# Kernel tuning notes

Measured on AMD Instinct MI355X. Metric: run time of the kernel, lower is better.

Reference implementation:

```python
import jax, jax.numpy as jnp
import numpy as np

N_NODES = 50000
N_EDGES = 800000
D_IN = 96
D_OUT = 96


def setup_inputs() -> dict:
    key = jax.random.key(0)
    k1, k2, k3 = jax.random.split(key, 3)
    x = jax.random.normal(k1, (N_NODES, D_IN), dtype=jnp.float32)
    edge_index = jax.random.randint(k2, (2, N_EDGES), 0, N_NODES, dtype=jnp.int64)
    edge_weight = jnp.ones((N_EDGES,), dtype=jnp.float32)
    # Glorot-ish init for the linear weight, zero bias (as in PyG GCNConv)
    W = jax.random.normal(k3, (D_IN, D_OUT), dtype=jnp.float32) * (1.0 / np.sqrt(D_IN))
    b = jnp.zeros((D_OUT,), dtype=jnp.float32)
    return {"x": x, "edge_index": edge_index, "edge_weight": edge_weight, "W": W, "b": b}


def reference(x, edge_index, edge_weight, W, b):
    """PyG GCNConv: out = D^{-1/2} (A + I) D^{-1/2} (x @ W) + b."""
    N = x.shape[0]
    row, col = edge_index[0], edge_index[1]  # source -> target
    # add self loops with weight 1 (PyG default add_self_loops=True)
    loop = jnp.arange(N, dtype=edge_index.dtype)
    row = jnp.concatenate([row, loop])
    col = jnp.concatenate([col, loop])
    ew = jnp.concatenate([edge_weight, jnp.ones((N,), dtype=edge_weight.dtype)])
    # symmetric normalization based on (weighted) in-degree over col
    deg = jax.ops.segment_sum(ew, col, num_segments=N)  # [N]
    dinv = jnp.where(deg > 0, jax.lax.rsqrt(deg), 0.0)
    norm = dinv[row] * ew * dinv[col]  # [E+N]
    # linear transform first (small GEMM), then gather-scale-scatter over edges
    h = x @ W  # [N, D_OUT]
    msg = h[row] * norm[:, None]  # [E+N, D_OUT]
    out = jax.ops.segment_sum(msg, col, num_segments=N)  # [N, D_OUT]
    return out + b
```

## Files before the change

### kernel.cpp

```cpp
#include <hip/hip_runtime.h>

#define N_NODES 50000
#define N_EDGES 800000
#define D 96
#define NBKT 256
#define BNODES 196
#define BCAP 4608
#define PART_B 250
#define EPB (N_EDGES / PART_B)
#define EPT 13
#define CAP 48
#define NSLOT (BNODES * CAP)
#define KDUMP 37
#define GCAP 768

typedef float vfloat4 __attribute__((ext_vector_type(4)));

__device__ __forceinline__ float bf_lo(unsigned u) { return __uint_as_float(u << 16); }
__device__ __forceinline__ float bf_hi(unsigned u) { return __uint_as_float(u & 0xFFFF0000u); }
__device__ __forceinline__ unsigned f2bf_bits(unsigned u) {
    return (u + 0x7FFFu + ((u >> 16) & 1u)) & 0xFFFF0000u;
}

__device__ __forceinline__ int exscan256(int v, int* wsum) {
    int lane = threadIdx.x & 63;
    int wave = threadIdx.x >> 6;
    int incl = v;
#pragma unroll
    for (int off = 1; off < 64; off <<= 1) {
        int t = __shfl_up(incl, off);
        if (lane >= off) incl += t;
    }
    if (lane == 63) wsum[wave] = incl;
    __syncthreads();
    int base = 0;
#pragma unroll
    for (int wv = 0; wv < 3; ++wv) base += (wv < wave) ? wsum[wv] : 0;
    return base + incl - v;
}

__global__ __launch_bounds__(256) void k_part(const int* __restrict__ row,
                                              const int* __restrict__ col,
                                              const float* __restrict__ ew,
                                              int* __restrict__ bkt_cnt,
                                              uint2* __restrict__ bktbuf) {
    __shared__ int hist[NBKT];
    __shared__ int cur[NBKT];
    int tid = threadIdx.x;
    hist[tid] = 0;
    __syncthreads();
    int e0 = blockIdx.x * EPB;

    int myc[EPT];
#pragma unroll
    for (int k = 0; k < EPT; ++k) {
        int i = tid + 256 * k;
        myc[k] = (i < EPB) ? col[e0 + i] : -1;
    }
#pragma unroll
    for (int k = 0; k < EPT; ++k)
        if (myc[k] >= 0) atomicAdd(&hist[myc[k] / BNODES], 1);
    __syncthreads();
    cur[tid] = atomicAdd(&bkt_cnt[tid], hist[tid]);
    __syncthreads();
#pragma unroll
    for (int k = 0; k < EPT; ++k) {
        int i = tid + 256 * k;
        if (myc[k] >= 0) {
            int e = e0 + i;
            int c = myc[k];
            int b = c / BNODES;
            int p = atomicAdd(&cur[b], 1);
            if (p < BCAP)
                bktbuf[(size_t)b * BCAP + p] =
                    make_uint2((unsigned)row[e] | ((unsigned)(c - b * BNODES) << 16),
                               __float_as_uint(ew[e]));
        }
    }
}

__global__ __launch_bounds__(256) void k_bin(const int* __restrict__ bkt_cnt,
                                             const uint2* __restrict__ bktbuf,
                                             unsigned* __restrict__ recs,
                                             int* __restrict__ rowptr,
                                             float* __restrict__ dinv) {
    __shared__ int wsum1[4];
    __shared__ int wsum2[4];
    __shared__ int sbkt[NBKT];
    __shared__ int lcnt[BNODES];
    __shared__ int loff[256];
    __shared__ int stot;
    __shared__ unsigned lslot[NSLOT];
    int tid = threadIdx.x;
    int b = blockIdx.x;

    int bv = min(bkt_cnt[tid], BCAP);
    int bex = exscan256(bv, wsum1);
    sbkt[tid] = bex;
    for (int i = tid; i < BNODES; i += 256) lcnt[i] = 0;
    __syncthreads();
    int gbase = sbkt[b];
    int ne = min(bkt_cnt[b], BCAP);

    for (int i = tid; i < ne; i += 256) {
        uint2 r = bktbuf[(size_t)b * BCAP + i];
        int lc = (int)(r.x >> 16);
        int p = atomicAdd(&lcnt[lc], 1);
        if (p < CAP) lslot[lc * CAP + p] = f2bf_bits(r.y) | (r.x & 0xFFFFu);
    }
    __syncthreads();

    int myv = (tid < BNODES) ? min(lcnt[tid], CAP) : 0;
    int ex2 = exscan256(myv, wsum2);
    loff[tid] = ex2;
    if (tid == 255) stot = ex2;
    __syncthreads();

    unsigned vals[KDUMP];
    int dst[KDUMP];
#pragma unroll
    for (int k = 0; k < KDUMP; ++k) {
        int i = tid + 256 * k;
        bool in = i < NSLOT;
        int ln = in ? i / CAP : 0;
        int s = in ? i % CAP : 0;
        bool act = in && (s < min(lcnt[ln], CAP));
        vals[k] = act ? lslot[i] : 0u;
        dst[k] = act ? (loff[ln] + s) : -1;
    }
    __syncthreads();
#pragma unroll
    for (int k = 0; k < KDUMP; ++k)
        if (dst[k] >= 0) lslot[dst[k]] = vals[k];
    __syncthreads();

    int tot = stot;
    for (int i = tid; i < tot; i += 256) recs[gbase + i] = lslot[i];

    int base = b * BNODES;
    for (int i = tid; i < BNODES; i += 256) {
        int n = base + i;
        if (n <= N_NODES) rowptr[n] = gbase + loff[i];
        if (n < N_NODES) {
            int cn = min(lcnt[i], CAP);
            int o = loff[i];
            float d = 1.0f;
            for (int k = 0; k < cn; ++k) d += bf_hi(lslot[o + k]);
            dinv[n] = rsqrtf(d);
        }
    }
}

__global__ __launch_bounds__(256) void k_gemm(const float* __restrict__ x,
                                              const float* __restrict__ W,
                                              const float* __restrict__ dinv,
                                              unsigned short* __restrict__ hb) {
    __shared__ float Wl[D * D];
    int tid = threadIdx.x;
    const float4* Wg4 = (const float4*)W;
    float4* Wl4 = (float4*)Wl;
    for (int i = tid; i < D * D / 4; i += 256) Wl4[i] = Wg4[i];
    __syncthreads();

    int jg = tid % 24;
    int ng = tid / 24;
    bool active = (ng < 10);
    int j = jg * 4;
    int node0 = blockIdx.x * 40 + ng * 4;

    float acc[4][4] = {};
    if (active) {
        for (int k4 = 0; k4 < D / 4; ++k4) {
            vfloat4 xv[4];
#pragma unroll
            for (int i = 0; i < 4; ++i)
                xv[i] = __builtin_nontemporal_load(
                    (const vfloat4*)&x[(node0 + i) * D + k4 * 4]);
#pragma unroll
            for (int kk = 0; kk < 4; ++kk) {
                float4 w4 = *(const float4*)&Wl[(k4 * 4 + kk) * D + j];
#pragma unroll
                for (int i = 0; i < 4; ++i) {
                    float xs = (kk == 0) ? xv[i].x : (kk == 1) ? xv[i].y
                             : (kk == 2) ? xv[i].z : xv[i].w;
                    acc[i][0] += xs * w4.x;
                    acc[i][1] += xs * w4.y;
                    acc[i][2] += xs * w4.z;
                    acc[i][3] += xs * w4.w;
                }
            }
        }
#pragma unroll
        for (int i = 0; i < 4; ++i) {
            int n = node0 + i;
            float di = dinv[n];
            ushort4 pk;
            pk.x = (unsigned short)(f2bf_bits(__float_as_uint(acc[i][0] * di)) >> 16);
            pk.y = (unsigned short)(f2bf_bits(__float_as_uint(acc[i][1] * di)) >> 16);
            pk.z = (unsigned short)(f2bf_bits(__float_as_uint(acc[i][2] * di)) >> 16);
            pk.w = (unsigned short)(f2bf_bits(__float_as_uint(acc[i][3] * di)) >> 16);
            *(ushort4*)&hb[(size_t)n * D + j] = pk;
        }
    }
}

__global__ __launch_bounds__(192) void k_gather(const int* __restrict__ rowptr,
                                                const unsigned* __restrict__ recs,
                                                const unsigned short* __restrict__ hb,
                                                const float* __restrict__ dinv,
                                                const float* __restrict__ bias,
                                                float* __restrict__ out) {
    __shared__ unsigned sre[GCAP];
    __shared__ int sptr[17];
    int tid = threadIdx.x;
    int nb = blockIdx.x * 16;

    if (tid < 17) sptr[tid] = rowptr[nb + tid];
    __syncthreads();
    int e0 = sptr[0];
    int stage = sptr[16] - e0;
    for (int i = tid; i < stage; i += 192) sre[i] = recs[e0 + i];
    __syncthreads();

    int local = tid / 12;
    int jq = tid % 12;
    int n = nb + local;
    int j = jq * 8;

    uint4 sv = *(const uint4*)(hb + (size_t)n * D + j);
    float acc[8];
    acc[0] = bf_lo(sv.x); acc[1] = bf_hi(sv.x);
    acc[2] = bf_lo(sv.y); acc[3] = bf_hi(sv.y);
    acc[4] = bf_lo(sv.z); acc[5] = bf_hi(sv.z);
    acc[6] = bf_lo(sv.w); acc[7] = bf_hi(sv.w);

    int ls = sptr[local] - e0;
    int le = sptr[local + 1] - e0;
    int idx = ls;
    for (; idx + 4 <= le; idx += 4) {
        unsigned r0 = sre[idx], r1 = sre[idx + 1], r2 = sre[idx + 2], r3 = sre[idx + 3];
        uint4 v0 = *(const uint4*)(hb + (size_t)(r0 & 0xFFFFu) * D + j);
        uint4 v1 = *(const uint4*)(hb + (size_t)(r1 & 0xFFFFu) * D + j);
        uint4 v2 = *(const uint4*)(hb + (size_t)(r2 & 0xFFFFu) * D + j);
        uint4 v3 = *(const uint4*)(hb + (size_t)(r3 & 0xFFFFu) * D + j);
        float w0 = bf_hi(r0), w1 = bf_hi(r1), w2 = bf_hi(r2), w3 = bf_hi(r3);
        acc[0] += w0 * bf_lo(v0.x); acc[1] += w0 * bf_hi(v0.x);
        acc[2] += w0 * bf_lo(v0.y); acc[3] += w0 * bf_hi(v0.y);
        acc[4] += w0 * bf_lo(v0.z); acc[5] += w0 * bf_hi(v0.z);
        acc[6] += w0 * bf_lo(v0.w); acc[7] += w0 * bf_hi(v0.w);
        acc[0] += w1 * bf_lo(v1.x); acc[1] += w1 * bf_hi(v1.x);
        acc[2] += w1 * bf_lo(v1.y); acc[3] += w1 * bf_hi(v1.y);
        acc[4] += w1 * bf_lo(v1.z); acc[5] += w1 * bf_hi(v1.z);
        acc[6] += w1 * bf_lo(v1.w); acc[7] += w1 * bf_hi(v1.w);
        acc[0] += w2 * bf_lo(v2.x); acc[1] += w2 * bf_hi(v2.x);
        acc[2] += w2 * bf_lo(v2.y); acc[3] += w2 * bf_hi(v2.y);
        acc[4] += w2 * bf_lo(v2.z); acc[5] += w2 * bf_hi(v2.z);
        acc[6] += w2 * bf_lo(v2.w); acc[7] += w2 * bf_hi(v2.w);
        acc[0] += w3 * bf_lo(v3.x); acc[1] += w3 * bf_hi(v3.x);
        acc[2] += w3 * bf_lo(v3.y); acc[3] += w3 * bf_hi(v3.y);
        acc[4] += w3 * bf_lo(v3.z); acc[5] += w3 * bf_hi(v3.z);
        acc[6] += w3 * bf_lo(v3.w); acc[7] += w3 * bf_hi(v3.w);
    }
    for (; idx < le; ++idx) {
        unsigned r0 = sre[idx];
        uint4 v0 = *(const uint4*)(hb + (size_t)(r0 & 0xFFFFu) * D + j);
        float w0 = bf_hi(r0);
        acc[0] += w0 * bf_lo(v0.x); acc[1] += w0 * bf_hi(v0.x);
        acc[2] += w0 * bf_lo(v0.y); acc[3] += w0 * bf_hi(v0.y);
        acc[4] += w0 * bf_lo(v0.z); acc[5] += w0 * bf_hi(v0.z);
        acc[6] += w0 * bf_lo(v0.w); acc[7] += w0 * bf_hi(v0.w);
    }

    float di = dinv[n];
    float4 b0 = *(const float4*)&bias[j];
    float4 b1 = *(const float4*)&bias[j + 4];
    vfloat4 o0, o1;
    o0.x = acc[0] * di + b0.x; o0.y = acc[1] * di + b0.y;
    o0.z = acc[2] * di + b0.z; o0.w = acc[3] * di + b0.w;
    o1.x = acc[4] * di + b1.x; o1.y = acc[5] * di + b1.y;
    o1.z = acc[6] * di + b1.z; o1.w = acc[7] * di + b1.w;
    __builtin_nontemporal_store(o0, (vfloat4*)&out[(size_t)n * D + j]);
    __builtin_nontemporal_store(o1, (vfloat4*)&out[(size_t)n * D + j + 4]);
}

extern "C" void kernel_launch(void* const* d_in, const int* in_sizes, int n_in,
                              void* d_out, int out_size, void* d_ws, size_t ws_size,
                              hipStream_t stream) {
    const float* x  = (const float*)d_in[0];
    const int*   ei = (const int*)d_in[1];
    const float* ew = (const float*)d_in[2];
    const float* W  = (const float*)d_in[3];
    const float* b  = (const float*)d_in[4];
    float* out = (float*)d_out;

    const int* row = ei;
    const int* col = ei + N_EDGES;

    char* p = (char*)d_ws;
    unsigned short* hb     = (unsigned short*)p;
    uint2*          bktbuf = (uint2*)p;            p += (size_t)N_NODES * D * 2;
    unsigned*       recs   = (unsigned*)p;         p += (size_t)N_EDGES * 4;
    int*            rowptr = (int*)p;              p += (size_t)(N_NODES + 16) * 4;
    float*          dinv   = (float*)p;            p += (size_t)N_NODES * 4;
    int*            bkt_cnt= (int*)p;              p += (size_t)NBKT * 4;

    (void)hipMemsetAsync(bkt_cnt, 0, NBKT * sizeof(int), stream);
    k_part  <<<PART_B, 256, 0, stream>>>(row, col, ew, bkt_cnt, bktbuf);
    k_bin   <<<NBKT, 256, 0, stream>>>(bkt_cnt, bktbuf, recs, rowptr, dinv);
    k_gemm  <<<1250, 256, 0, stream>>>(x, W, dinv, hb);
    k_gather<<<(N_NODES + 15) / 16, 192, 0, stream>>>(rowptr, recs, hb, dinv, b, out);
}
```

Measured before the change: 157.4 us.

## Double bucket count and write CSR records directly from padded slots

Raises the bucket count from 256 to 512 with half as many nodes per bucket, so the binning kernel runs twice as many blocks, each with a smaller shared-memory footprint. The in-LDS compaction pass, which staged records in registers and needed extra barriers, is removed. Each slot is now written straight to its final global position, and degrees are summed from the padded slot layout. This trades contiguous coalesced global writes for scattered ones and needs more partition atomics per block. The GEMM changes are only cleanup.

```diff
diff --git a/kernel.cpp b/kernel.cpp
--- a/kernel.cpp
+++ b/kernel.cpp
@@ -3,15 +3,14 @@
 #define N_NODES 50000
 #define N_EDGES 800000
 #define D 96
-#define NBKT 256
-#define BNODES 196
-#define BCAP 4608
+#define NBKT 512
+#define BNODES 98
+#define BCAP 2304
 #define PART_B 250
-#define EPB (N_EDGES / PART_B)
+#define EPB 3200
 #define EPT 13
 #define CAP 48
 #define NSLOT (BNODES * CAP)
-#define KDUMP 37
 #define GCAP 768
 
 typedef float vfloat4 __attribute__((ext_vector_type(4)));
@@ -20,6 +19,9 @@
 __device__ __forceinline__ float bf_hi(unsigned u) { return __uint_as_float(u & 0xFFFF0000u); }
 __device__ __forceinline__ unsigned f2bf_bits(unsigned u) {
     return (u + 0x7FFFu + ((u >> 16) & 1u)) & 0xFFFF0000u;
+}
+__device__ __forceinline__ unsigned short f2bf16(float f) {
+    return (unsigned short)(f2bf_bits(__float_as_uint(f)) >> 16);
 }
 
 __device__ __forceinline__ int exscan256(int v, int* wsum) {
@@ -48,9 +50,9 @@
     __shared__ int cur[NBKT];
     int tid = threadIdx.x;
     hist[tid] = 0;
+    hist[tid + 256] = 0;
     __syncthreads();
     int e0 = blockIdx.x * EPB;
-
     int myc[EPT];
 #pragma unroll
     for (int k = 0; k < EPT; ++k) {
@@ -62,6 +64,7 @@
         if (myc[k] >= 0) atomicAdd(&hist[myc[k] / BNODES], 1);
     __syncthreads();
     cur[tid] = atomicAdd(&bkt_cnt[tid], hist[tid]);
+    cur[tid + 256] = atomicAdd(&bkt_cnt[tid + 256], hist[tid + 256]);
     __syncthreads();
 #pragma unroll
     for (int k = 0; k < EPT; ++k) {
@@ -89,15 +92,16 @@
     __shared__ int sbkt[NBKT];
     __shared__ int lcnt[BNODES];
     __shared__ int loff[256];
-    __shared__ int stot;
     __shared__ unsigned lslot[NSLOT];
     int tid = threadIdx.x;
     int b = blockIdx.x;
 
-    int bv = min(bkt_cnt[tid], BCAP);
-    int bex = exscan256(bv, wsum1);
-    sbkt[tid] = bex;
-    for (int i = tid; i < BNODES; i += 256) lcnt[i] = 0;
+    int c0 = min(bkt_cnt[2 * tid], BCAP);
+    int c1 = min(bkt_cnt[2 * tid + 1], BCAP);
+    int ps = exscan256(c0 + c1, wsum1);
+    sbkt[2 * tid] = ps;
+    sbkt[2 * tid + 1] = ps + c0;
+    if (tid < BNODES) lcnt[tid] = 0;
     __syncthreads();
     int gbase = sbkt[b];
     int ne = min(bkt_cnt[b], BCAP);
@@ -113,39 +117,21 @@
     int myv = (tid < BNODES) ? min(lcnt[tid], CAP) : 0;
     int ex2 = exscan256(myv, wsum2);
     loff[tid] = ex2;
-    if (tid == 255) stot = ex2;
-    __syncthreads();
-
-    unsigned vals[KDUMP];
-    int dst[KDUMP];
-#pragma unroll
-    for (int k = 0; k < KDUMP; ++k) {
-        int i = tid + 256 * k;
-        bool in = i < NSLOT;
-        int ln = in ? i / CAP : 0;
-        int s = in ? i % CAP : 0;
-        bool act = in && (s < min(lcnt[ln], CAP));
-        vals[k] = act ? lslot[i] : 0u;
-        dst[k] = act ? (loff[ln] + s) : -1;
-    }
-    __syncthreads();
-#pragma unroll
-    for (int k = 0; k < KDUMP; ++k)
-        if (dst[k] >= 0) lslot[dst[k]] = vals[k];
-    __syncthreads();
-
-    int tot = stot;
-    for (int i = tid; i < tot; i += 256) recs[gbase + i] = lslot[i];
-
+    __syncthreads();
+
+    for (int i = tid; i < NSLOT; i += 256) {
+        int ln = i / CAP, s = i % CAP;
+        if (s < min(lcnt[ln], CAP))
+            recs[gbase + loff[ln] + s] = lslot[i];
+    }
     int base = b * BNODES;
-    for (int i = tid; i < BNODES; i += 256) {
-        int n = base + i;
-        if (n <= N_NODES) rowptr[n] = gbase + loff[i];
+    if (tid < BNODES) {
+        int n = base + tid;
+        if (n <= N_NODES) rowptr[n] = gbase + loff[tid];
         if (n < N_NODES) {
-            int cn = min(lcnt[i], CAP);
-            int o = loff[i];
+            int cn = min(lcnt[tid], CAP);
             float d = 1.0f;
-            for (int k = 0; k < cn; ++k) d += bf_hi(lslot[o + k]);
+            for (int k = 0; k < cn; ++k) d += bf_hi(lslot[tid * CAP + k]);
             dinv[n] = rsqrtf(d);
         }
     }
@@ -164,43 +150,41 @@
 
     int jg = tid % 24;
     int ng = tid / 24;
-    bool active = (ng < 10);
+    if (ng >= 10) return;
     int j = jg * 4;
     int node0 = blockIdx.x * 40 + ng * 4;
 
     float acc[4][4] = {};
-    if (active) {
-        for (int k4 = 0; k4 < D / 4; ++k4) {
-            vfloat4 xv[4];
-#pragma unroll
-            for (int i = 0; i < 4; ++i)
-                xv[i] = __builtin_nontemporal_load(
-                    (const vfloat4*)&x[(node0 + i) * D + k4 * 4]);
-#pragma unroll
-            for (int kk = 0; kk < 4; ++kk) {
-                float4 w4 = *(const float4*)&Wl[(k4 * 4 + kk) * D + j];
-#pragma unroll
-                for (int i = 0; i < 4; ++i) {
-                    float xs = (kk == 0) ? xv[i].x : (kk == 1) ? xv[i].y
-                             : (kk == 2) ? xv[i].z : xv[i].w;
-                    acc[i][0] += xs * w4.x;
-                    acc[i][1] += xs * w4.y;
-                    acc[i][2] += xs * w4.z;
-                    acc[i][3] += xs * w4.w;
-                }
+    for (int k4 = 0; k4 < D / 4; ++k4) {
+        vfloat4 xv[4];
+#pragma unroll
+        for (int i = 0; i < 4; ++i)
+            xv[i] = __builtin_nontemporal_load(
+                (const vfloat4*)&x[(node0 + i) * D + k4 * 4]);
+#pragma unroll
+        for (int kk = 0; kk < 4; ++kk) {
+            float4 w4 = *(const float4*)&Wl[(k4 * 4 + kk) * D + j];
+#pragma unroll
+            for (int i = 0; i < 4; ++i) {
+                float xs = (kk == 0) ? xv[i].x : (kk == 1) ? xv[i].y
+                         : (kk == 2) ? xv[i].z : xv[i].w;
+                acc[i][0] += xs * w4.x;
+                acc[i][1] += xs * w4.y;
+                acc[i][2] += xs * w4.z;
+                acc[i][3] += xs * w4.w;
             }
         }
-#pragma unroll
-        for (int i = 0; i < 4; ++i) {
-            int n = node0 + i;
-            float di = dinv[n];
-            ushort4 pk;
-            pk.x = (unsigned short)(f2bf_bits(__float_as_uint(acc[i][0] * di)) >> 16);
-            pk.y = (unsigned short)(f2bf_bits(__float_as_uint(acc[i][1] * di)) >> 16);
-            pk.z = (unsigned short)(f2bf_bits(__float_as_uint(acc[i][2] * di)) >> 16);
-            pk.w = (unsigned short)(f2bf_bits(__float_as_uint(acc[i][3] * di)) >> 16);
-            *(ushort4*)&hb[(size_t)n * D + j] = pk;
-        }
+    }
+#pragma unroll
+    for (int i = 0; i < 4; ++i) {
+        int n = node0 + i;
+        float di = dinv[n];
+        ushort4 pk;
+        pk.x = f2bf16(acc[i][0] * di);
+        pk.y = f2bf16(acc[i][1] * di);
+        pk.z = f2bf16(acc[i][2] * di);
+        pk.w = f2bf16(acc[i][3] * di);
+        *(ushort4*)&hb[(size_t)n * D + j] = pk;
     }
 }
 
```

Result: faster. 152.4 us (median of 2 runs) (-3.1%).
